# Kernel optimization log

Hardware: AMD Instinct MI355X
Metric: run time of the kernel (lower is better)

The kernel has to match this reference:

```python
import jax, jax.numpy as jnp
import numpy as np

N = 4096   # num_nodes == nb_items
E = 3      # num_edge types
C = 2      # num_channels
D = 128    # basket_embed_dim
RU = 128   # rnn_units
B = 32     # batch size
L = 20     # max_seq_length
ALPHA = 0.5


def _gtconv(W, A):
    # softmax over edge types, then channel-weighted combine of adjacencies
    f = jax.nn.softmax(W, axis=1)              # [C, E]
    return jnp.einsum('ce,enm->cnm', f, A)     # [C, N, N]


def _normalize(H):
    # remove self loops, then column-degree (in-degree) inverse normalization
    eye = jnp.eye(H.shape[-1], dtype=H.dtype)
    Hn = H * (1.0 - eye)
    deg = Hn.sum(axis=1)                        # scatter_add over col -> [C, N]
    dinv = jnp.where(deg == 0, jnp.zeros_like(deg), 1.0 / deg)
    dinv = jax.lax.stop_gradient(dinv)          # original computes deg under no_grad
    return Hn * dinv[:, None, :]


def _lstm(x, h0, c0, W_ih, W_hh, b_ih, b_hh):
    # single-layer batch-first LSTM, torch gate order (i, f, g, o)
    def step(carry, xt):
        h, c = carry
        z = xt @ W_ih.T + b_ih + h @ W_hh.T + b_hh
        i, f, g, o = jnp.split(z, 4, axis=-1)
        c = jax.nn.sigmoid(f) * c + jax.nn.sigmoid(i) * jnp.tanh(g)
        h = jax.nn.sigmoid(o) * jnp.tanh(c)
        return (h, c), h
    _, ys = jax.lax.scan(step, (h0, c0), jnp.swapaxes(x, 0, 1))
    return jnp.swapaxes(ys, 0, 1)               # [B, L, RU]


def setup_inputs():
    key = jax.random.key(0)
    k = jax.random.split(key, 12)
    A = jax.random.uniform(k[0], (E, N, N), jnp.float32) * (2.0 / N)
    seqs = (jax.random.uniform(k[1], (B, L, N)) < 0.02).astype(jnp.float32)
    seq_len = jax.random.randint(k[2], (B,), 1, L + 1)
    h0 = jnp.zeros((B, RU), jnp.float32)
    c0 = jnp.zeros((B, RU), jnp.float32)
    W1a = 1.0 + 0.1 * jax.random.normal(k[3], (C, E), jnp.float32)
    W1b = 1.0 + 0.1 * jax.random.normal(k[4], (C, E), jnp.float32)
    W2 = 1.0 + 0.1 * jax.random.normal(k[5], (C, E), jnp.float32)
    I_B = jnp.ones((N,), jnp.float32) / N
    lin_w = jax.random.normal(k[6], (C, D, N), jnp.float32) / np.sqrt(N).astype(np.float32)
    lin_b = jnp.zeros((C, D), jnp.float32)
    proj_w = jax.random.normal(k[7], (D, C * D), jnp.float32) / np.sqrt(C * D).astype(np.float32)
    proj_b = jnp.zeros((D,), jnp.float32)
    W_ih = jax.random.normal(k[8], (4 * RU, D), jnp.float32) / np.sqrt(D).astype(np.float32)
    W_hh = jax.random.normal(k[9], (4 * RU, RU), jnp.float32) / np.sqrt(RU).astype(np.float32)
    b_ih = jnp.zeros((4 * RU,), jnp.float32)
    b_hh = jnp.zeros((4 * RU,), jnp.float32)
    h2item_w = jax.random.normal(k[10], (N, RU), jnp.float32) / np.sqrt(RU).astype(np.float32)
    return dict(A=A, seqs=seqs, seq_len=seq_len, h0=h0, c0=c0, W1a=W1a, W1b=W1b,
                W2=W2, I_B=I_B, lin_w=lin_w, lin_b=lin_b, proj_w=proj_w, proj_b=proj_b,
                W_ih=W_ih, W_hh=W_hh, b_ih=b_ih, b_hh=b_hh, h2item_w=h2item_w)


def reference(A, seqs, seq_len, h0, c0, W1a, W1b, W2, I_B, lin_w, lin_b,
              proj_w, proj_b, W_ih, W_hh, b_ih, b_hh, h2item_w):
    # layer 0 (first=True): H[c] = conv1(A)[c] @ conv2(A)[c]  (spspmm, dense form)
    H = jnp.einsum('cij,cjk->cik', _gtconv(W1a, A), _gtconv(W1b, A))
    # layer 1: H[c] = norm(H)[c] @ conv(A)[c]
    H = jnp.einsum('cij,cjk->cik', _normalize(H), _gtconv(W2, A))

    x = seqs.reshape(-1, N)                     # [B*L, nb_items]
    v = jax.nn.relu(I_B)                        # diag(I_B) after relu
    enc = []
    for i in range(C):
        xh = jax.nn.relu(x @ H[i])
        if i == 0:
            e = jax.nn.relu(x * v) + xh         # note: channel-0 formula differs
        else:
            e = jax.nn.relu(x * v + xh)
        enc.append(e @ lin_w[i].T + lin_b[i])
    enc = jnp.concatenate(enc, axis=1)          # [B*L, C*D]
    baskets = (enc @ proj_w.T + proj_b).reshape(B, L, D)

    lstm_out = _lstm(baskets, h0, c0, W_ih, W_hh, b_ih, b_hh)
    idx = jnp.arange(B) * L + (seq_len - 1)
    last = lstm_out.reshape(-1, RU)[idx]        # [B, RU]
    probs = jax.nn.sigmoid(last @ h2item_w.T)   # [B, nb_items]
    return (1.0 - ALPHA) * probs + ALPHA * (probs * v)
```

## Files before the change

### kernel.cpp

```cpp
#include <hip/hip_runtime.h>


typedef float  f4v  __attribute__((ext_vector_type(4)));
typedef short  s8v  __attribute__((ext_vector_type(8)));
typedef unsigned short u16;
typedef u16    us4  __attribute__((ext_vector_type(4)));
typedef unsigned int u32;
typedef u32    u2v  __attribute__((ext_vector_type(2)));
typedef u32    u4v  __attribute__((ext_vector_type(4)));

#define NN 4096
#define MM 640

__device__ __forceinline__ u16 f2bf(float f){
  unsigned int u = __float_as_uint(f);
  u += 0x7FFFu + ((u>>16)&1u);
  return (u16)(u>>16);
}
__device__ __forceinline__ float bf2f(u16 h){ return __uint_as_float(((unsigned int)h)<<16); }
__device__ __forceinline__ float sigm(float x){ return 1.f/(1.f+__expf(-x)); }

__device__ __forceinline__ u32 pkbf(float lo, float hi){
  u32 r;
  asm("v_cvt_pk_bf16_f32 %0, %1, %2" : "=v"(r) : "v"(lo), "v"(hi));
  return r;
}

__device__ __forceinline__ void gload16(const void* g, void* l){
  __builtin_amdgcn_global_load_lds((const __attribute__((address_space(1))) unsigned int*)g,
                                   (__attribute__((address_space(3))) unsigned int*)l, 16, 0, 0);
}

__device__ __forceinline__ void softmax23(const float* __restrict__ W, float f[2][3]){
  #pragma unroll
  for (int c=0;c<2;c++){
    float a=W[c*3+0], b=W[c*3+1], d=W[c*3+2];
    float m=fmaxf(a,fmaxf(b,d));
    float ea=__expf(a-m), eb=__expf(b-m), ed=__expf(d-m);
    float s=1.f/(ea+eb+ed);
    f[c][0]=ea*s; f[c][1]=eb*s; f[c][2]=ed*s;
  }
}

__global__ __launch_bounds__(256)
void k_combine_all(const float* __restrict__ A, const float* __restrict__ W1a,
                   const float* __restrict__ W1b, const float* __restrict__ W2,
                   u16* __restrict__ C1, u16* __restrict__ C2t,
                   u16* __restrict__ C3t, float* __restrict__ r)
{
  __shared__ u16 t2[2][64][68];
  __shared__ u16 t3[2][64][68];
  __shared__ float rs[2][64];
  const int tid = threadIdx.x, lane = tid&63;
  const int n0 = blockIdx.x*64, m0 = blockIdx.y*64;
  float fa[2][3], fb[2][3], fc[2][3];
  softmax23(W1a, fa); softmax23(W1b, fb); softmax23(W2, fc);
  if (tid < 128) rs[tid>>6][tid&63] = 0.f;
  __syncthreads();
  const int mb = tid>>4, nb = tid&15;
  f4v a0[4], a1[4], a2[4];
  #pragma unroll
  for (int j=0;j<4;j++){
    const float* ap = A + (size_t)(m0+mb*4+j)*NN + n0 + nb*4;
    a0[j] = *(const f4v*)ap;
    a1[j] = *(const f4v*)(ap + (size_t)NN*NN);
    a2[j] = *(const f4v*)(ap + 2*(size_t)NN*NN);
  }
  float rp[2][4] = {};
  #pragma unroll
  for (int c=0;c<2;c++){
    f4v v1[4], vt[4], v3[4];
    #pragma unroll
    for (int j=0;j<4;j++){
      v1[j] = fa[c][0]*a0[j] + fa[c][1]*a1[j] + fa[c][2]*a2[j];
      vt[j] = fb[c][0]*a0[j] + fb[c][1]*a1[j] + fb[c][2]*a2[j];
      v3[j] = fc[c][0]*a0[j] + fc[c][1]*a1[j] + fc[c][2]*a2[j];
    }
    #pragma unroll
    for (int j=0;j<4;j++){
      u2v o = { pkbf(v1[j][0],v1[j][1]), pkbf(v1[j][2],v1[j][3]) };
      *(u2v*)(C1 + ((size_t)c*NN + m0+mb*4+j)*NN + n0 + nb*4) = o;
      #pragma unroll
      for (int k=0;k<4;k++) rp[c][k] += v1[j][k];
    }
    #pragma unroll
    for (int jj=0;jj<4;jj++){
      u2v o2 = { pkbf(vt[0][jj],vt[1][jj]), pkbf(vt[2][jj],vt[3][jj]) };
      u2v o3 = { pkbf(v3[0][jj],v3[1][jj]), pkbf(v3[2][jj],v3[3][jj]) };
      *(u2v*)&t2[c][nb*4+jj][mb*4] = o2;
      *(u2v*)&t3[c][nb*4+jj][mb*4] = o3;
    }
  }
  #pragma unroll
  for (int c=0;c<2;c++)
    #pragma unroll
    for (int k=0;k<4;k++){
      float v = rp[c][k];
      v += __shfl_xor(v,16); v += __shfl_xor(v,32);
      if (lane < 16) atomicAdd(&rs[c][(lane&15)*4+k], v);
    }
  __syncthreads();
  if (tid < 128) atomicAdd(&r[(size_t)(tid>>6)*NN + n0 + (tid&63)], rs[tid>>6][tid&63]);
  const int nl = tid>>2, mc = tid&3;
  #pragma unroll
  for (int c=0;c<2;c++){
    #pragma unroll
    for (int rep=0;rep<2;rep++){
      const int cc = mc + rep*4;
      u2v lo2 = *(const u2v*)&t2[c][nl][cc*8];
      u2v hi2 = *(const u2v*)&t2[c][nl][cc*8+4];
      u4v o2 = { lo2[0], lo2[1], hi2[0], hi2[1] };
      *(u4v*)(C2t + ((size_t)c*NN + n0+nl)*NN + m0 + cc*8) = o2;
      u2v lo3 = *(const u2v*)&t3[c][nl][cc*8];
      u2v hi3 = *(const u2v*)&t3[c][nl][cc*8+4];
      u4v o3 = { lo3[0], lo3[1], hi3[0], hi3[1] };
      *(u4v*)(C3t + ((size_t)c*NN + n0+nl)*NN + m0 + cc*8) = o3;
    }
  }
}

__global__ __launch_bounds__(256)
void k_sparse_y(const float* __restrict__ seqs, const u16* __restrict__ C1,
                u16* __restrict__ y)
{
  __shared__ int idxl[512];
  __shared__ int cnt;
  const int tid = threadIdx.x, row = blockIdx.x;
  if (tid==0) cnt = 0;
  __syncthreads();
  const float* xr = seqs + (size_t)row*NN;
  #pragma unroll
  for (int it=0; it<4; ++it){
    f4v v = *(const f4v*)(xr + it*1024 + tid*4);
    #pragma unroll
    for (int k=0;k<4;k++) if (v[k] > 0.5f){ int p = atomicAdd(&cnt,1); if (p<512) idxl[p] = it*1024+tid*4+k; }
  }
  __syncthreads();
  const int nz = cnt < 512 ? cnt : 512;
  float acc0[16], acc1[16];
  #pragma unroll
  for (int k=0;k<16;k++){ acc0[k]=0.f; acc1[k]=0.f; }
  const int cb = tid*16;
  s8v ca, cb8, cc8, cd8;
  if (nz > 0){
    const u16* r0 = C1 + (size_t)idxl[0]*NN + cb;
    const u16* r1 = r0 + (size_t)NN*NN;
    ca=*(const s8v*)r0; cb8=*(const s8v*)(r0+8); cc8=*(const s8v*)r1; cd8=*(const s8v*)(r1+8);
  }
  for (int p=0;p<nz;++p){
    const int pn = (p+1<nz)? p+1 : p;
    const u16* r0 = C1 + (size_t)idxl[pn]*NN + cb;
    const u16* r1 = r0 + (size_t)NN*NN;
    s8v na=*(const s8v*)r0, nb=*(const s8v*)(r0+8), nc=*(const s8v*)r1, nd=*(const s8v*)(r1+8);
    #pragma unroll
    for (int k=0;k<8;k++){
      acc0[k]   += bf2f((u16)ca[k]);
      acc0[8+k] += bf2f((u16)cb8[k]);
      acc1[k]   += bf2f((u16)cc8[k]);
      acc1[8+k] += bf2f((u16)cd8[k]);
    }
    ca=na; cb8=nb; cc8=nc; cd8=nd;
  }
  u4v o0, o1;
  #pragma unroll
  for (int k=0;k<4;k++){
    o0[k] = pkbf(acc0[2*k], acc0[2*k+1]);
    o1[k] = pkbf(acc0[8+2*k], acc0[9+2*k]);
  }
  u16* y0 = y + (size_t)row*NN + cb;
  *(u4v*)y0 = o0; *(u4v*)(y0+8) = o1;
  #pragma unroll
  for (int k=0;k<4;k++){
    o0[k] = pkbf(acc1[2*k], acc1[2*k+1]);
    o1[k] = pkbf(acc1[8+2*k], acc1[9+2*k]);
  }
  u16* y1 = y0 + (size_t)MM*NN;
  *(u4v*)y1 = o0; *(u4v*)(y1+8) = o1;
}

__global__ __launch_bounds__(256)
void k_diagdeg(const u16* __restrict__ C1, const u16* __restrict__ C2t,
               const float* __restrict__ r, float* __restrict__ diag1,
               float* __restrict__ dinv)
{
  const int tid = threadIdx.x, lane = tid&63;
  const int gw = blockIdx.x*4 + (tid>>6);
  const int c = gw>>12, k = gw&4095;
  const u16* p1 = C1  + ((size_t)c*NN + k)*NN;
  const u16* p2 = C2t + ((size_t)c*NN + k)*NN;
  const float* pr = r + (size_t)c*NN;
  float dd = 0.f, dg = 0.f;
  for (int it=0; it<8; ++it){
    const int j = it*512 + lane*8;
    s8v v1 = *(const s8v*)(p1+j);
    s8v v2 = *(const s8v*)(p2+j);
    f4v r0 = *(const f4v*)(pr+j);
    f4v r1 = *(const f4v*)(pr+j+4);
    #pragma unroll
    for (int q=0;q<8;q++){
      float c2 = bf2f((u16)v2[q]);
      dd += bf2f((u16)v1[q]) * c2;
      dg += ((q<4)? r0[q] : r1[q-4]) * c2;
    }
  }
  #pragma unroll
  for (int m=1;m<64;m<<=1){ dd += __shfl_xor(dd, m); dg += __shfl_xor(dg, m); }
  if (lane==0){
    float deg = dg - dd;
    diag1[(size_t)c*NN+k] = dd;
    dinv[(size_t)c*NN+k]  = (deg==0.f) ? 0.f : 1.f/deg;
  }
}

template<int EPI>
__global__ __launch_bounds__(256)
void k_gemmf(const u16* __restrict__ Xb, const u16* __restrict__ Bt,
             const float* __restrict__ seqs, const float* __restrict__ diag1,
             const float* __restrict__ dinv, const float* __restrict__ IB,
             u16* __restrict__ outp)
{
  __shared__ u16 As[64*64];
  __shared__ u16 Bs[64*64];
  const int tid = threadIdx.x, lane = tid&63, w = tid>>6;
  const int m0 = blockIdx.x*64, n0 = blockIdx.y*64;
  const int c = blockIdx.z;
  const u16* Ab = Xb + (size_t)c*MM*NN;
  const u16* Bb = Bt + (size_t)c*NN*NN;
  const int srow = lane>>3;
  const int scol = ((lane&7) ^ (srow&7))*8;
  const int fr = lane&15, fkq = lane>>4;
  const int wm = (w>>1)*32, wn = (w&1)*32;
  f4v acc[2][2] = {};
  for (int k0=0;k0<NN;k0+=64){
    #pragma unroll
    for (int t=0;t<2;t++){
      gload16(Ab + (size_t)(m0 + t*32 + w*8 + srow)*NN + k0 + scol, (void*)&As[(t*32 + w*8)*64]);
      gload16(Bb + (size_t)(n0 + t*32 + w*8 + srow)*NN + k0 + scol, (void*)&Bs[(t*32 + w*8)*64]);
    }
    __syncthreads();
    #pragma unroll
    for (int kk=0;kk<2;kk++){
      s8v a[2], b[2];
      #pragma unroll
      for (int t=0;t<2;t++){
        const int ra = wm + t*16 + fr;
        a[t] = *(const s8v*)&As[ra*64 + (((kk*4 + fkq) ^ (ra&7))*8)];
        const int rb = wn + t*16 + fr;
        b[t] = *(const s8v*)&Bs[rb*64 + (((kk*4 + fkq) ^ (rb&7))*8)];
      }
      #pragma unroll
      for (int i=0;i<2;i++)
        #pragma unroll
        for (int j=0;j<2;j++)
          acc[i][j] = __builtin_amdgcn_mfma_f32_16x16x32_bf16(a[i], b[j], acc[i][j], 0, 0, 0);
    }
    __syncthreads();
  }
  #pragma unroll
  for (int i=0;i<2;i++){
    #pragma unroll
    for (int j=0;j<2;j++){
      const int col = n0 + wn + j*16 + fr;
      float dg, dv, vv;
      if constexpr(EPI==0){ dg = diag1[(size_t)c*NN+col]; dv = dinv[(size_t)c*NN+col]; }
      else                { vv = fmaxf(IB[col], 0.f); }
      #pragma unroll
      for (int rr=0;rr<4;rr++){
        const int row = m0 + wm + i*16 + (lane>>4)*4 + rr;
        const float z = acc[i][j][rr];
        const float x = seqs[(size_t)row*NN + col];
        float val;
        if constexpr(EPI==0){
          val = (z - x*dg) * dv;
        } else {
          float xh = fmaxf(z, 0.f);
          val = (c==0) ? (fmaxf(x*vv,0.f) + xh) : fmaxf(x*vv + xh, 0.f);
        }
        outp[((size_t)c*MM + row)*NN + col] = f2bf(val);
      }
    }
  }
}

__global__ __launch_bounds__(256)
void k_cvt(const float* __restrict__ linw, const float* __restrict__ whh,
           u16* __restrict__ linwb, u16* __restrict__ whhb)
{
  const int g = blockIdx.x*256 + threadIdx.x;
  const int i = g*4;
  const int NL = 2*128*NN;
  f4v v; u16* dst;
  if (i < NL){ v = *(const f4v*)(linw + i); dst = linwb + i; }
  else       { v = *(const f4v*)(whh + (i-NL)); dst = whhb + (i-NL); }
  u2v o = { pkbf(v[0],v[1]), pkbf(v[2],v[3]) };
  *(u2v*)dst = o;
}

__global__ __launch_bounds__(256)
void k_lin(const u16* __restrict__ e, const u16* __restrict__ linwb,
           float* __restrict__ encr)
{
  __shared__ u16 As[64*32];
  __shared__ u16 Bs[64*32];
  const int tid=threadIdx.x, lane=tid&63, w=tid>>6;
  const int m0 = blockIdx.x*64, d0 = blockIdx.y*64;
  const int c = blockIdx.z>>4, ks = blockIdx.z&15;
  const u16* Ab = e + (size_t)c*MM*NN;
  const u16* Bb = linwb + (size_t)c*128*NN;
  const int srow=lane>>2, skof=(lane&3)*8, fr=lane&15, fk=(lane>>4)*8;
  const int wm=(w>>1)*32, wn=(w&1)*32;
  f4v acc[2][2];
  #pragma unroll
  for (int i=0;i<2;i++)
    #pragma unroll
    for (int j=0;j<2;j++) acc[i][j] = (f4v){0.f,0.f,0.f,0.f};
  for (int ki=0;ki<8;++ki){
    const int k0 = ks*256 + ki*32;
    gload16(Ab + (size_t)(m0 + w*16 + srow)*NN + k0 + skof, (void*)&As[(w*16)*32]);
    gload16(Bb + (size_t)(d0 + w*16 + srow)*NN + k0 + skof, (void*)&Bs[(w*16)*32]);
    __syncthreads();
    s8v a[2], b[2];
    #pragma unroll
    for (int t=0;t<2;t++) a[t] = *(const s8v*)&As[(wm+t*16+fr)*32+fk];
    #pragma unroll
    for (int t=0;t<2;t++) b[t] = *(const s8v*)&Bs[(wn+t*16+fr)*32+fk];
    #pragma unroll
    for (int i=0;i<2;i++)
      #pragma unroll
      for (int j=0;j<2;j++)
        acc[i][j] = __builtin_amdgcn_mfma_f32_16x16x32_bf16(a[i], b[j], acc[i][j], 0, 0, 0);
    __syncthreads();
  }
  #pragma unroll
  for (int i=0;i<2;i++)
    #pragma unroll
    for (int j=0;j<2;j++){
      const int col = d0 + wn + j*16 + fr;
      #pragma unroll
      for (int rr=0;rr<4;rr++){
        const int row = m0 + wm + i*16 + (lane>>4)*4 + rr;
        atomicAdd(&encr[(size_t)row*256 + c*128 + col], acc[i][j][rr]);
      }
    }
}

__global__ __launch_bounds__(256)
void k_proj(const float* __restrict__ encr, const float* __restrict__ linb,
            const float* __restrict__ pw, const float* __restrict__ pb,
            float* __restrict__ bask)
{
  const int g = blockIdx.x*256 + threadIdx.x;
  const int row = g>>7, d = g&127;
  const float* er = encr + (size_t)row*256;
  const float* wr = pw + (size_t)d*256;
  float acc = pb[d];
  for (int j=0;j<256;j+=4){
    f4v e4 = *(const f4v*)(er+j);
    f4v l4 = *(const f4v*)(linb+j);
    f4v w4 = *(const f4v*)(wr+j);
    acc += (e4[0]+l4[0])*w4[0] + (e4[1]+l4[1])*w4[1] + (e4[2]+l4[2])*w4[2] + (e4[3]+l4[3])*w4[3];
  }
  bask[g] = acc;
}

__global__ __launch_bounds__(256)
void k_xhat(const float* __restrict__ bask, const float* __restrict__ wih,
            const float* __restrict__ bih, const float* __restrict__ bhh,
            float* __restrict__ xh)
{
  const int g = blockIdx.x*256 + threadIdx.x;
  const int row = g>>9, n = g&511;
  const float* br = bask + (size_t)row*128;
  const float* wr = wih + (size_t)n*128;
  float acc = bih[n] + bhh[n];
  for (int k=0;k<128;k+=4){
    f4v b4=*(const f4v*)(br+k); f4v w4=*(const f4v*)(wr+k);
    acc += b4[0]*w4[0]+b4[1]*w4[1]+b4[2]*w4[2]+b4[3]*w4[3];
  }
  const int b = row/20, t = row%20;
  xh[((size_t)t*32 + b)*512 + n] = acc;
}

__global__ __launch_bounds__(512)
void k_lstm(const float* __restrict__ xhat, const u16* __restrict__ whhb,
            const float* __restrict__ h0, const float* __restrict__ c0,
            const int* __restrict__ slen, float* __restrict__ last)
{
  __shared__ float zb[32][512];
  __shared__ float cbuf[32][128];
  __shared__ u16 hb[32][136];
  const int tid = threadIdx.x, lane = tid&63, w = tid>>6;
  for (int i=tid; i<4096; i+=512){ int b=i>>7,u=i&127; cbuf[b][u]=c0[i]; hb[b][u]=f2bf(h0[i]); }
  const int fr = lane&15, fko = (lane>>4)*8;
  s8v bfr[4][4];
  #pragma unroll
  for (int nt=0;nt<4;nt++)
    #pragma unroll
    for (int kf=0;kf<4;kf++)
      bfr[nt][kf] = *(const s8v*)(whhb + (size_t)(w*64 + nt*16 + fr)*128 + kf*32 + fko);
  __syncthreads();
  for (int t=0;t<20;++t){
    s8v af[2][4];
    #pragma unroll
    for (int mt=0;mt<2;mt++)
      #pragma unroll
      for (int kf=0;kf<4;kf++)
        af[mt][kf] = *(const s8v*)&hb[mt*16+fr][kf*32+fko];
    f4v z[2][4];
    #pragma unroll
    for (int mt=0;mt<2;mt++)
      #pragma unroll
      for (int nt=0;nt<4;nt++){
        const int nn2 = w*64 + nt*16 + fr;
        #pragma unroll
        for (int rr=0;rr<4;rr++){
          const int bb = mt*16 + (lane>>4)*4 + rr;
          z[mt][nt][rr] = xhat[((size_t)t*32 + bb)*512 + nn2];
        }
      }
    #pragma unroll
    for (int kf=0;kf<4;kf++)
      #pragma unroll
      for (int mt=0;mt<2;mt++)
        #pragma unroll
        for (int nt=0;nt<4;nt++)
          z[mt][nt] = __builtin_amdgcn_mfma_f32_16x16x32_bf16(af[mt][kf], bfr[nt][kf], z[mt][nt], 0, 0, 0);
    #pragma unroll
    for (int mt=0;mt<2;mt++)
      #pragma unroll
      for (int nt=0;nt<4;nt++){
        const int nn2 = w*64 + nt*16 + fr;
        #pragma unroll
        for (int rr=0;rr<4;rr++){
          const int bb = mt*16 + (lane>>4)*4 + rr;
          zb[bb][nn2] = z[mt][nt][rr];
        }
      }
    __syncthreads();
    for (int p=tid; p<4096; p+=512){
      const int b=p>>7, u=p&127;
      float zi=zb[b][u], zf=zb[b][128+u], zg=zb[b][256+u], zo=zb[b][384+u];
      float ii=sigm(zi), ff=sigm(zf), gg=tanhf(zg), oo=sigm(zo);
      float cn = ff*cbuf[b][u] + ii*gg;
      float hn = oo*tanhf(cn);
      cbuf[b][u]=cn; hb[b][u]=f2bf(hn);
      if (t == slen[b]-1) last[p] = hn;
    }
    __syncthreads();
  }
}

__global__ __launch_bounds__(256)
void k_final(const float* __restrict__ last, const float* __restrict__ h2w,
             const float* __restrict__ IB, float* __restrict__ out)
{
  __shared__ float ls[128];
  const int b = blockIdx.y;
  const int n = blockIdx.x*256 + threadIdx.x;
  if (threadIdx.x < 128) ls[threadIdx.x] = last[b*128 + threadIdx.x];
  __syncthreads();
  const float* wr = h2w + (size_t)n*128;
  float acc = 0.f;
  for (int k=0;k<128;k+=4){
    f4v w4 = *(const f4v*)(wr+k);
    acc += w4[0]*ls[k] + w4[1]*ls[k+1] + w4[2]*ls[k+2] + w4[3]*ls[k+3];
  }
  const float vn = fmaxf(IB[n], 0.f);
  out[(size_t)b*NN + n] = (0.5f + 0.5f*vn) * sigm(acc);
}

extern "C" void kernel_launch(void* const* d_in, const int* in_sizes, int n_in,
                              void* d_out, int out_size, void* d_ws, size_t ws_size,
                              hipStream_t stream)
{
  const float* A    = (const float*)d_in[0];
  const float* seqs = (const float*)d_in[1];
  const int*   slen = (const int*)  d_in[2];
  const float* h0   = (const float*)d_in[3];
  const float* c0   = (const float*)d_in[4];
  const float* W1a  = (const float*)d_in[5];
  const float* W1b  = (const float*)d_in[6];
  const float* W2   = (const float*)d_in[7];
  const float* IB   = (const float*)d_in[8];
  const float* linw = (const float*)d_in[9];
  const float* linb = (const float*)d_in[10];
  const float* pw   = (const float*)d_in[11];
  const float* pb   = (const float*)d_in[12];
  const float* wih  = (const float*)d_in[13];
  const float* whh  = (const float*)d_in[14];
  const float* bih  = (const float*)d_in[15];
  const float* bhh  = (const float*)d_in[16];
  const float* h2w  = (const float*)d_in[17];
  (void)in_sizes; (void)n_in; (void)out_size; (void)ws_size;

  char* ws = (char*)d_ws;
  size_t off = 0;
  auto alloc = [&](size_t sz)->void*{ void* p = ws + off; off += (sz + 255) & ~(size_t)255; return p; };
  u16*   C1    = (u16*)  alloc((size_t)2*NN*NN*2);
  u16*   C2t   = (u16*)  alloc((size_t)2*NN*NN*2);
  u16*   C3t   = (u16*)  alloc((size_t)2*NN*NN*2);
  u16*   y     = (u16*)  alloc((size_t)2*MM*NN*2);
  u16*   u     = (u16*)  alloc((size_t)2*MM*NN*2);
  float* r     = (float*)alloc((size_t)2*NN*4);
  float* diag1 = (float*)alloc((size_t)2*NN*4);
  float* dinv  = (float*)alloc((size_t)2*NN*4);
  u16*   linwb = (u16*)  alloc((size_t)2*128*NN*2);
  u16*   whhb  = (u16*)  alloc((size_t)512*128*2);
  float* encr  = (float*)alloc((size_t)MM*256*4);
  float* bask  = (float*)alloc((size_t)MM*128*4);
  float* xh    = (float*)alloc((size_t)20*32*512*4);
  float* last  = (float*)alloc((size_t)32*128*4);

  hipMemsetAsync(r, 0, (size_t)2*NN*4, stream);
  hipMemsetAsync(encr, 0, (size_t)MM*256*4, stream);

  k_combine_all<<<dim3(64,64),256,0,stream>>>(A, W1a, W1b, W2, C1, C2t, C3t, r);
  k_sparse_y<<<MM,256,0,stream>>>(seqs, C1, y);
  k_diagdeg<<<2048,256,0,stream>>>(C1, C2t, r, diag1, dinv);
  k_gemmf<0><<<dim3(10,64,2),256,0,stream>>>(y, C2t, seqs, diag1, dinv, IB, u);
  u16* e = y;
  k_gemmf<1><<<dim3(10,64,2),256,0,stream>>>(u, C3t, seqs, diag1, dinv, IB, e);
  k_cvt<<<1088,256,0,stream>>>(linw, whh, linwb, whhb);
  k_lin<<<dim3(10,2,32),256,0,stream>>>(e, linwb, encr);
  k_proj<<<320,256,0,stream>>>(encr, linb, pw, pb, bask);
  k_xhat<<<1280,256,0,stream>>>(bask, wih, bih, bhh, xh);
  k_lstm<<<1,512,0,stream>>>(xh, whhb, h0, c0, slen, last);
  k_final<<<dim3(16,32),256,0,stream>>>(last, h2w, IB, (float*)d_out);
}
```

Baseline: 549.4 us.

## Double-buffer GEMM LDS, split sparse_y columns, restructure combine kernel

Adds LDS double buffering to the bf16 GEMM so the next K-tile's global loads overlap MFMA work. Splits the sparse row-accumulation kernel over two column halves to double block count and cut registers. Restructures the adjacency-combine kernel to process half-rows and one channel at a time with smaller LDS tiles, which lowers register and LDS use but rereads A from global memory for the transposed outputs.

New measurement: 662.7 us. 20.6% more time.

```diff
diff --git a/kernel.cpp b/kernel.cpp
--- a/kernel.cpp
+++ b/kernel.cpp
@@ -4,7 +4,6 @@
 typedef float  f4v  __attribute__((ext_vector_type(4)));
 typedef short  s8v  __attribute__((ext_vector_type(8)));
 typedef unsigned short u16;
-typedef u16    us4  __attribute__((ext_vector_type(4)));
 typedef unsigned int u32;
 typedef u32    u2v  __attribute__((ext_vector_type(2)));
 typedef u32    u4v  __attribute__((ext_vector_type(4)));
@@ -48,73 +47,80 @@
                    u16* __restrict__ C1, u16* __restrict__ C2t,
                    u16* __restrict__ C3t, float* __restrict__ r)
 {
-  __shared__ u16 t2[2][64][68];
-  __shared__ u16 t3[2][64][68];
+  __shared__ u16 t2[64][72];
+  __shared__ u16 t3[64][72];
   __shared__ float rs[2][64];
   const int tid = threadIdx.x, lane = tid&63;
   const int n0 = blockIdx.x*64, m0 = blockIdx.y*64;
   float fa[2][3], fb[2][3], fc[2][3];
   softmax23(W1a, fa); softmax23(W1b, fb); softmax23(W2, fc);
   if (tid < 128) rs[tid>>6][tid&63] = 0.f;
-  __syncthreads();
   const int mb = tid>>4, nb = tid&15;
-  f4v a0[4], a1[4], a2[4];
-  #pragma unroll
-  for (int j=0;j<4;j++){
-    const float* ap = A + (size_t)(m0+mb*4+j)*NN + n0 + nb*4;
-    a0[j] = *(const f4v*)ap;
-    a1[j] = *(const f4v*)(ap + (size_t)NN*NN);
-    a2[j] = *(const f4v*)(ap + 2*(size_t)NN*NN);
-  }
   float rp[2][4] = {};
   #pragma unroll
-  for (int c=0;c<2;c++){
-    f4v v1[4], vt[4], v3[4];
-    #pragma unroll
-    for (int j=0;j<4;j++){
-      v1[j] = fa[c][0]*a0[j] + fa[c][1]*a1[j] + fa[c][2]*a2[j];
-      vt[j] = fb[c][0]*a0[j] + fb[c][1]*a1[j] + fb[c][2]*a2[j];
-      v3[j] = fc[c][0]*a0[j] + fc[c][1]*a1[j] + fc[c][2]*a2[j];
-    }
-    #pragma unroll
-    for (int j=0;j<4;j++){
-      u2v o = { pkbf(v1[j][0],v1[j][1]), pkbf(v1[j][2],v1[j][3]) };
-      *(u2v*)(C1 + ((size_t)c*NN + m0+mb*4+j)*NN + n0 + nb*4) = o;
-      #pragma unroll
-      for (int k=0;k<4;k++) rp[c][k] += v1[j][k];
-    }
-    #pragma unroll
-    for (int jj=0;jj<4;jj++){
-      u2v o2 = { pkbf(vt[0][jj],vt[1][jj]), pkbf(vt[2][jj],vt[3][jj]) };
-      u2v o3 = { pkbf(v3[0][jj],v3[1][jj]), pkbf(v3[2][jj],v3[3][jj]) };
-      *(u2v*)&t2[c][nb*4+jj][mb*4] = o2;
-      *(u2v*)&t3[c][nb*4+jj][mb*4] = o3;
-    }
-  }
+  for (int h=0;h<2;h++){
+    f4v a0[2], a1[2], a2[2];
+    #pragma unroll
+    for (int j=0;j<2;j++){
+      const float* ap = A + (size_t)(m0+mb*4+2*h+j)*NN + n0 + nb*4;
+      a0[j] = *(const f4v*)ap;
+      a1[j] = *(const f4v*)(ap + (size_t)NN*NN);
+      a2[j] = *(const f4v*)(ap + 2*(size_t)NN*NN);
+    }
+    #pragma unroll
+    for (int c=0;c<2;c++){
+      #pragma unroll
+      for (int j=0;j<2;j++){
+        f4v v1 = fa[c][0]*a0[j] + fa[c][1]*a1[j] + fa[c][2]*a2[j];
+        u2v o = { pkbf(v1[0],v1[1]), pkbf(v1[2],v1[3]) };
+        *(u2v*)(C1 + ((size_t)c*NN + m0+mb*4+2*h+j)*NN + n0 + nb*4) = o;
+        #pragma unroll
+        for (int k=0;k<4;k++) rp[c][k] += v1[k];
+      }
+    }
+  }
+  __syncthreads();
   #pragma unroll
   for (int c=0;c<2;c++)
     #pragma unroll
     for (int k=0;k<4;k++){
       float v = rp[c][k];
       v += __shfl_xor(v,16); v += __shfl_xor(v,32);
-      if (lane < 16) atomicAdd(&rs[c][(lane&15)*4+k], v);
+      if (lane < 16) atomicAdd(&rs[c][nb*4+k], v);
     }
   __syncthreads();
   if (tid < 128) atomicAdd(&r[(size_t)(tid>>6)*NN + n0 + (tid&63)], rs[tid>>6][tid&63]);
-  const int nl = tid>>2, mc = tid&3;
   #pragma unroll
   for (int c=0;c<2;c++){
+    __syncthreads();
+    #pragma unroll
+    for (int h=0;h<2;h++){
+      f4v a0[2], a1[2], a2[2];
+      #pragma unroll
+      for (int j=0;j<2;j++){
+        const float* ap = A + (size_t)(m0+mb*4+2*h+j)*NN + n0 + nb*4;
+        a0[j] = *(const f4v*)ap;
+        a1[j] = *(const f4v*)(ap + (size_t)NN*NN);
+        a2[j] = *(const f4v*)(ap + 2*(size_t)NN*NN);
+      }
+      f4v vt[2], v3[2];
+      #pragma unroll
+      for (int j=0;j<2;j++){
+        vt[j] = fb[c][0]*a0[j] + fb[c][1]*a1[j] + fb[c][2]*a2[j];
+        v3[j] = fc[c][0]*a0[j] + fc[c][1]*a1[j] + fc[c][2]*a2[j];
+      }
+      #pragma unroll
+      for (int jj=0;jj<4;jj++){
+        *(u32*)&t2[nb*4+jj][mb*4+2*h] = pkbf(vt[0][jj], vt[1][jj]);
+        *(u32*)&t3[nb*4+jj][mb*4+2*h] = pkbf(v3[0][jj], v3[1][jj]);
+      }
+    }
+    __syncthreads();
     #pragma unroll
     for (int rep=0;rep<2;rep++){
-      const int cc = mc + rep*4;
-      u2v lo2 = *(const u2v*)&t2[c][nl][cc*8];
-      u2v hi2 = *(const u2v*)&t2[c][nl][cc*8+4];
-      u4v o2 = { lo2[0], lo2[1], hi2[0], hi2[1] };
-      *(u4v*)(C2t + ((size_t)c*NN + n0+nl)*NN + m0 + cc*8) = o2;
-      u2v lo3 = *(const u2v*)&t3[c][nl][cc*8];
-      u2v hi3 = *(const u2v*)&t3[c][nl][cc*8+4];
-      u4v o3 = { lo3[0], lo3[1], hi3[0], hi3[1] };
-      *(u4v*)(C3t + ((size_t)c*NN + n0+nl)*NN + m0 + cc*8) = o3;
+      const int rw = rep*32 + (tid>>3), l8 = tid&7;
+      *(u4v*)(C2t + ((size_t)c*NN + n0+rw)*NN + m0 + l8*8) = *(const u4v*)&t2[rw][l8*8];
+      *(u4v*)(C3t + ((size_t)c*NN + n0+rw)*NN + m0 + l8*8) = *(const u4v*)&t3[rw][l8*8];
     }
   }
 }
@@ -137,45 +143,36 @@
   }
   __syncthreads();
   const int nz = cnt < 512 ? cnt : 512;
-  float acc0[16], acc1[16];
-  #pragma unroll
-  for (int k=0;k<16;k++){ acc0[k]=0.f; acc1[k]=0.f; }
-  const int cb = tid*16;
-  s8v ca, cb8, cc8, cd8;
+  float acc0[8], acc1[8];
+  #pragma unroll
+  for (int k=0;k<8;k++){ acc0[k]=0.f; acc1[k]=0.f; }
+  const int cb = blockIdx.y*2048 + tid*8;
+  s8v ca, cc8;
   if (nz > 0){
     const u16* r0 = C1 + (size_t)idxl[0]*NN + cb;
-    const u16* r1 = r0 + (size_t)NN*NN;
-    ca=*(const s8v*)r0; cb8=*(const s8v*)(r0+8); cc8=*(const s8v*)r1; cd8=*(const s8v*)(r1+8);
+    ca  = *(const s8v*)r0;
+    cc8 = *(const s8v*)(r0 + (size_t)NN*NN);
   }
   for (int p=0;p<nz;++p){
     const int pn = (p+1<nz)? p+1 : p;
     const u16* r0 = C1 + (size_t)idxl[pn]*NN + cb;
-    const u16* r1 = r0 + (size_t)NN*NN;
-    s8v na=*(const s8v*)r0, nb=*(const s8v*)(r0+8), nc=*(const s8v*)r1, nd=*(const s8v*)(r1+8);
+    s8v na = *(const s8v*)r0;
+    s8v nc = *(const s8v*)(r0 + (size_t)NN*NN);
     #pragma unroll
     for (int k=0;k<8;k++){
-      acc0[k]   += bf2f((u16)ca[k]);
-      acc0[8+k] += bf2f((u16)cb8[k]);
-      acc1[k]   += bf2f((u16)cc8[k]);
-      acc1[8+k] += bf2f((u16)cd8[k]);
-    }
-    ca=na; cb8=nb; cc8=nc; cd8=nd;
+      acc0[k] += bf2f((u16)ca[k]);
+      acc1[k] += bf2f((u16)cc8[k]);
+    }
+    ca=na; cc8=nc;
   }
   u4v o0, o1;
   #pragma unroll
   for (int k=0;k<4;k++){
     o0[k] = pkbf(acc0[2*k], acc0[2*k+1]);
-    o1[k] = pkbf(acc0[8+2*k], acc0[9+2*k]);
-  }
-  u16* y0 = y + (size_t)row*NN + cb;
-  *(u4v*)y0 = o0; *(u4v*)(y0+8) = o1;
-  #pragma unroll
-  for (int k=0;k<4;k++){
-    o0[k] = pkbf(acc1[2*k], acc1[2*k+1]);
-    o1[k] = pkbf(acc1[8+2*k], acc1[9+2*k]);
-  }
-  u16* y1 = y0 + (size_t)MM*NN;
-  *(u4v*)y1 = o0; *(u4v*)(y1+8) = o1;
+    o1[k] = pkbf(acc1[2*k], acc1[2*k+1]);
+  }
+  *(u4v*)(y + (size_t)row*NN + cb) = o0;
+  *(u4v*)(y + (size_t)MM*NN + (size_t)row*NN + cb) = o1;
 }
 
 __global__ __launch_bounds__(256)
@@ -219,8 +216,8 @@
              const float* __restrict__ dinv, const float* __restrict__ IB,
              u16* __restrict__ outp)
 {
-  __shared__ u16 As[64*64];
-  __shared__ u16 Bs[64*64];
+  __shared__ u16 As[2][64*64];
+  __shared__ u16 Bs[2][64*64];
   const int tid = threadIdx.x, lane = tid&63, w = tid>>6;
   const int m0 = blockIdx.x*64, n0 = blockIdx.y*64;
   const int c = blockIdx.z;
@@ -231,22 +228,27 @@
   const int fr = lane&15, fkq = lane>>4;
   const int wm = (w>>1)*32, wn = (w&1)*32;
   f4v acc[2][2] = {};
+  auto STAGE = [&](int buf, int k0){
+    #pragma unroll
+    for (int t=0;t<2;t++){
+      gload16(Ab + (size_t)(m0 + t*32 + w*8 + srow)*NN + k0 + scol, (void*)&As[buf][(t*32 + w*8)*64]);
+      gload16(Bb + (size_t)(n0 + t*32 + w*8 + srow)*NN + k0 + scol, (void*)&Bs[buf][(t*32 + w*8)*64]);
+    }
+  };
+  STAGE(0, 0);
+  __syncthreads();
+  int cur = 0;
   for (int k0=0;k0<NN;k0+=64){
-    #pragma unroll
-    for (int t=0;t<2;t++){
-      gload16(Ab + (size_t)(m0 + t*32 + w*8 + srow)*NN + k0 + scol, (void*)&As[(t*32 + w*8)*64]);
-      gload16(Bb + (size_t)(n0 + t*32 + w*8 + srow)*NN + k0 + scol, (void*)&Bs[(t*32 + w*8)*64]);
-    }
-    __syncthreads();
+    if (k0+64 < NN) STAGE(cur^1, k0+64);
     #pragma unroll
     for (int kk=0;kk<2;kk++){
       s8v a[2], b[2];
       #pragma unroll
       for (int t=0;t<2;t++){
         const int ra = wm + t*16 + fr;
-        a[t] = *(const s8v*)&As[ra*64 + (((kk*4 + fkq) ^ (ra&7))*8)];
+        a[t] = *(const s8v*)&As[cur][ra*64 + (((kk*4 + fkq) ^ (ra&7))*8)];
         const int rb = wn + t*16 + fr;
-        b[t] = *(const s8v*)&Bs[rb*64 + (((kk*4 + fkq) ^ (rb&7))*8)];
+        b[t] = *(const s8v*)&Bs[cur][rb*64 + (((kk*4 + fkq) ^ (rb&7))*8)];
       }
       #pragma unroll
       for (int i=0;i<2;i++)
@@ -255,6 +257,7 @@
           acc[i][j] = __builtin_amdgcn_mfma_f32_16x16x32_bf16(a[i], b[j], acc[i][j], 0, 0, 0);
     }
     __syncthreads();
+    cur ^= 1;
   }
   #pragma unroll
   for (int i=0;i<2;i++){
@@ -515,7 +518,7 @@
   hipMemsetAsync(encr, 0, (size_t)MM*256*4, stream);
 
   k_combine_all<<<dim3(64,64),256,0,stream>>>(A, W1a, W1b, W2, C1, C2t, C3t, r);
-  k_sparse_y<<<MM,256,0,stream>>>(seqs, C1, y);
+  k_sparse_y<<<dim3(MM,2),256,0,stream>>>(seqs, C1, y);
   k_diagdeg<<<2048,256,0,stream>>>(C1, C2t, r, diag1, dinv);
   k_gemmf<0><<<dim3(10,64,2),256,0,stream>>>(y, C2t, seqs, diag1, dinv, IB, u);
   u16* e = y;
```
